# Kernel tuning notes

Hardware: AMD Instinct MI355X
Metric: run time of the kernel (lower is better)

Reference implementation:

```python
import jax, jax.numpy as jnp
import numpy as np

N, D, K = 32768, 64, 8192

def setup_inputs() -> dict:
    key = jax.random.key(0)
    k1, k2 = jax.random.split(key)
    x = jax.random.normal(k1, (N, D), dtype=jnp.float32)
    w = jax.random.normal(k2, (D, K), dtype=jnp.float32)  # codebook: (embedding_dim, num_embeddings)
    return {"x": x, "w": w}

def reference(x, w):
    distances = (
        jnp.sum(x * x, axis=1, keepdims=True)
        - 2.0 * (x @ w)
        + jnp.sum(w * w, axis=0, keepdims=True)
    )  # [N, K]
    encoding_indices = jnp.argmin(distances, axis=1)  # [N] (argmax of -distances)
    # quantize: embedding_lookup on w^T  -> [N, D]
    quantized = jnp.take(w.T, encoding_indices, axis=0)
    return quantized
```

## Files before the change

kernel.cpp:

```cpp
#include <hip/hip_runtime.h>
#include <hip/hip_bf16.h>
#include <hip/hip_fp16.h>
#include <cstdint>
#include <cstddef>

#define NROWS 32768
#define DDIM  64
#define KDIM  8192
#define DELTA 1.25f

typedef float  f32x4 __attribute__((ext_vector_type(4)));
typedef short  s16x8 __attribute__((ext_vector_type(8)));
typedef unsigned long long u64;


__device__ __forceinline__ uint32_t fmono(float f) {
    uint32_t u = __float_as_uint(f);
    return (u & 0x80000000u) ? ~u : (u | 0x80000000u);
}


__global__ void __launch_bounds__(256)
vq_prep(const float* __restrict__ w, const float* __restrict__ x,
        ushort* __restrict__ wtb, float* __restrict__ wt,
        float4* __restrict__ wt4, float* __restrict__ wsq,
        ushort* __restrict__ xb) {
    __shared__ float tile[64][65];
    const int t = threadIdx.x, wv = t >> 6, lane = t & 63;
    const int l15 = lane & 15, l4 = (lane >> 4) & 3;

    if (blockIdx.x < KDIM / 64) {
        const int bid = blockIdx.x;
        const int kbase = bid * 64;
#pragma unroll
        for (int it = 0; it < 16; ++it) {
            int d = it * 4 + wv;
            tile[lane][d] = w[(size_t)d * KDIM + kbase + lane];
        }
        __syncthreads();
#pragma unroll
        for (int h = 0; h < 2; ++h) {
            s16x8 c;
#pragma unroll
            for (int e = 0; e < 8; ++e) {
                float v = -2.0f * tile[wv * 16 + l15][h * 32 + l4 * 8 + e];
                __hip_bfloat16 hb = __float2bfloat16(v);
                c[e] = *(short*)&hb;
            }
            ((s16x8*)wtb)[(size_t)(bid * 4 + wv) * 128 + h * 64 + lane] = c;
        }
#pragma unroll
        for (int it = 0; it < 16; ++it) {
            int kk = it * 4 + wv;
            wt[(size_t)(kbase + kk) * DDIM + lane] = tile[kk][lane];
        }
#pragma unroll
        for (int it = 0; it < 4; ++it) {
            int i = wv * 4 + it;
            float4 v;
            v.x = tile[lane][i * 4 + 0];
            v.y = tile[lane][i * 4 + 1];
            v.z = tile[lane][i * 4 + 2];
            v.w = tile[lane][i * 4 + 3];
            wt4[(size_t)i * KDIM + kbase + lane] = v;
        }
        if (wv == 0) {
            float s = 0.f;
#pragma unroll
            for (int d = 0; d < DDIM; ++d) {
                float v = tile[lane][d];
                s = fmaf(v, v, s);
            }
            wsq[kbase + lane] = s;
        }
    } else {
        const int bid = blockIdx.x - KDIM / 64;
        const int r = bid * 64 + wv * 16 + l15;
#pragma unroll
        for (int h = 0; h < 2; ++h) {
            const float* src = &x[(size_t)r * DDIM + h * 32 + l4 * 8];
            float4 a = *(const float4*)src;
            float4 b = *(const float4*)(src + 4);
            float fv[8] = {a.x, a.y, a.z, a.w, b.x, b.y, b.z, b.w};
            s16x8 c;
#pragma unroll
            for (int e = 0; e < 8; ++e) {
                __hip_bfloat16 hb = __float2bfloat16(fv[e]);
                c[e] = *(short*)&hb;
            }
            ((s16x8*)xb)[(size_t)(bid * 4 + wv) * 128 + h * 64 + lane] = c;
        }
    }
}

__global__ void __launch_bounds__(256)
vq_scoreA(const ushort* __restrict__ xb, const ushort* __restrict__ wb,
          const float* __restrict__ wsq, ushort* __restrict__ lsub) {
    const int t = threadIdx.x, wv = t >> 6, lane = t & 63;
    const int l15 = lane & 15, l4 = lane >> 4;
    const int rbase = (blockIdx.x & 255) * 128;
    const int kg    = (blockIdx.x >> 8) * 4 + wv;
    const int kbase = kg * 256;

    const s16x8* xs  = (const s16x8*)xb;
    const s16x8* wsx = (const s16x8*)wb;

    s16x8 bfrag[8][2];
#pragma unroll
    for (int rt = 0; rt < 8; ++rt)
#pragma unroll
        for (int h = 0; h < 2; ++h)
            bfrag[rt][h] = xs[(size_t)((rbase >> 4) + rt) * 128 + h * 64 + lane];

    u64 packs[8];
#pragma unroll
    for (int rt = 0; rt < 8; ++rt) packs[rt] = 0ull;

#pragma unroll
    for (int sub = 0; sub < 4; ++sub) {
        const int kw = kbase + sub * 64;

        s16x8 afrag[4][2];
#pragma unroll
        for (int kt = 0; kt < 4; ++kt)
#pragma unroll
            for (int h = 0; h < 2; ++h)
                afrag[kt][h] = wsx[(size_t)((kw >> 4) + kt) * 128 + h * 64 + lane];

        f32x4 wq[4];
#pragma unroll
        for (int kt = 0; kt < 4; ++kt)
            wq[kt] = *(const f32x4*)&wsq[kw + kt * 16 + l4 * 4];

#pragma unroll
        for (int rt = 0; rt < 8; ++rt) {
            f32x4 acc[4];
#pragma unroll
            for (int kt = 0; kt < 4; ++kt) acc[kt] = wq[kt];
#pragma unroll
            for (int kt = 0; kt < 4; ++kt) {
                acc[kt] = __builtin_amdgcn_mfma_f32_16x16x32_bf16(afrag[kt][0], bfrag[rt][0], acc[kt], 0, 0, 0);
                acc[kt] = __builtin_amdgcn_mfma_f32_16x16x32_bf16(afrag[kt][1], bfrag[rt][1], acc[kt], 0, 0, 0);
            }
            float g0 = fminf(fminf(acc[0][0], acc[0][1]), acc[0][2]);
            float g1 = fminf(fminf(acc[0][3], acc[1][0]), acc[1][1]);
            float g2 = fminf(fminf(acc[1][2], acc[1][3]), acc[2][0]);
            float g3 = fminf(fminf(acc[2][1], acc[2][2]), acc[2][3]);
            float g4 = fminf(fminf(acc[3][0], acc[3][1]), acc[3][2]);
            float h0 = fminf(fminf(g0, g1), g2);
            float h1 = fminf(fminf(g3, g4), acc[3][3]);
            float m  = fminf(h0, h1);
            m = fminf(m, __shfl_xor(m, 16));
            m = fminf(m, __shfl_xor(m, 32));
            __half hh = __float2half(m);
            packs[rt] |= (u64)(*(ushort*)&hh) << (16 * sub);
        }
    }

    if (l4 == 0) {
#pragma unroll
        for (int rt = 0; rt < 8; ++rt)
            *(u64*)&lsub[(size_t)(rbase + rt * 16 + l15) * 128 + kg * 4] = packs[rt];
    }
}

__global__ void __launch_bounds__(64)
vq_finish(const float* __restrict__ x, const float4* __restrict__ wt4,
          const float* __restrict__ wt, const float* __restrict__ wsq,
          const ushort* __restrict__ lsub, float* __restrict__ out) {
    const int lane = threadIdx.x;
    const int row  = blockIdx.x;

    ushort2 us = ((const ushort2*)(lsub + (size_t)row * 128))[lane];
    float v0 = __half2float(*(__half*)&us.x);
    float v1 = __half2float(*(__half*)&us.y);
    float m = fminf(v0, v1);
#pragma unroll
    for (int o = 1; o < 64; o <<= 1) m = fminf(m, __shfl_xor(m, o));
    const float thr = m + DELTA;
    u64 b0 = __ballot(v0 <= thr);
    u64 b1 = __ballot(v1 <= thr);

    float xs[64];
    const float4* xp = (const float4*)(x + (size_t)row * DDIM);
#pragma unroll
    for (int i = 0; i < 16; ++i) {
        float4 v = xp[i];
        xs[4 * i + 0] = v.x;
        xs[4 * i + 1] = v.y;
        xs[4 * i + 2] = v.z;
        xs[4 * i + 3] = v.w;
    }

    u64 best = ~0ull;
#pragma unroll
    for (int half = 0; half < 2; ++half) {
        u64 b = half ? b1 : b0;
        while (b) {
            int s = __ffsll(b) - 1;
            b &= b - 1;
            const int kk = (s * 2 + half) * 64 + lane;
            float qq = wsq[kk];
            const float4* wr = wt4 + kk;
            float a0 = 0.f, a1 = 0.f, a2 = 0.f, a3 = 0.f;
#pragma unroll
            for (int i = 0; i < 16; ++i) {
                float4 wv4 = wr[(size_t)i * KDIM];
                a0 = fmaf(xs[4 * i + 0], wv4.x, a0);
                a1 = fmaf(xs[4 * i + 1], wv4.y, a1);
                a2 = fmaf(xs[4 * i + 2], wv4.z, a2);
                a3 = fmaf(xs[4 * i + 3], wv4.w, a3);
            }
            float dot = (a0 + a1) + (a2 + a3);
            float sc  = fmaf(-2.f, dot, qq);
            u64 key = ((u64)fmono(sc) << 32) | (unsigned)kk;
            best = (key < best) ? key : best;
        }
    }
#pragma unroll
    for (int sh = 1; sh < 64; sh <<= 1) {
        u64 o = __shfl_xor(best, sh);
        best = (o < best) ? o : best;
    }
    const int bk = (int)(best & 0xFFFFFFFFull);
    out[(size_t)row * DDIM + lane] = wt[(size_t)bk * DDIM + lane];
}


#define BR 128
#define BK 128
#define DPH 32
typedef float v2f __attribute__((ext_vector_type(2)));

__global__ void fb_prep(const float* __restrict__ w, float* __restrict__ wt,
                        float* __restrict__ wsq) {
    int k = blockIdx.x * blockDim.x + threadIdx.x;
    if (k >= KDIM) return;
    float s = 0.f;
#pragma unroll
    for (int d = 0; d < DDIM; ++d) {
        float v = w[(size_t)d * KDIM + k];
        wt[(size_t)k * DDIM + d] = v;
        s = fmaf(v, v, s);
    }
    wsq[k] = s;
}
__global__ void fb_init(u64* __restrict__ keys) {
    int i = blockIdx.x * blockDim.x + threadIdx.x;
    if (i < NROWS) keys[i] = ~0ull;
}
__global__ void __launch_bounds__(256, 4)
fb_gemm(const float* __restrict__ x, const float* __restrict__ w,
        const float* __restrict__ wsq, u64* __restrict__ keys) {
    __shared__ float xT[DPH][BR];
    __shared__ float wl[DPH][BK];
    const int kblk  = blockIdx.x & (KDIM / BK - 1);
    const int rbase = (blockIdx.x >> 6) * BR;
    const int kbase = kblk * BK;
    const int t     = threadIdx.x;
    const int wave = t >> 6, lane = t & 63;
    const int rg = lane >> 3, cg = lane & 7;
    const int xoff = (wave >> 1) * 64 + rg * 8;
    const int coff = (wave & 1) * 64 + cg * 8;
    v2f acc[8][4];
#pragma unroll
    for (int i = 0; i < 8; ++i)
#pragma unroll
        for (int j = 0; j < 4; ++j) acc[i][j] = (v2f)(0.f);
#pragma unroll
    for (int p = 0; p < 2; ++p) {
        {
            const int row = t & 127, dgrp = t >> 7;
#pragma unroll
            for (int it = 0; it < 4; ++it) {
                const int dl = (dgrp + it * 2) * 4;
                float4 v = *(const float4*)&x[(size_t)(rbase + row) * DDIM + p * DPH + dl];
                xT[dl + 0][row] = v.x; xT[dl + 1][row] = v.y;
                xT[dl + 2][row] = v.z; xT[dl + 3][row] = v.w;
            }
        }
        {
#pragma unroll
            for (int it = 0; it < 4; ++it) {
                const int o4 = t + it * 256;
                const int dl = o4 >> 5, c4 = (o4 & 31) << 2;
                float4 v = *(const float4*)&w[(size_t)(p * DPH + dl) * KDIM + kbase + c4];
                *(float4*)&wl[dl][c4] = v;
            }
        }
        __syncthreads();
#pragma unroll 4
        for (int d = 0; d < DPH; ++d) {
            float4 xa = *(const float4*)&xT[d][xoff];
            float4 xb = *(const float4*)&xT[d][xoff + 4];
            float4 wa = *(const float4*)&wl[d][coff];
            float4 wb = *(const float4*)&wl[d][coff + 4];
            v2f wv0 = {wa.x, wa.y}, wv1 = {wa.z, wa.w};
            v2f wv2 = {wb.x, wb.y}, wv3 = {wb.z, wb.w};
            float xrr[8] = {xa.x, xa.y, xa.z, xa.w, xb.x, xb.y, xb.z, xb.w};
#pragma unroll
            for (int i = 0; i < 8; ++i) {
                v2f xsV = {xrr[i], xrr[i]};
                acc[i][0] = __builtin_elementwise_fma(xsV, wv0, acc[i][0]);
                acc[i][1] = __builtin_elementwise_fma(xsV, wv1, acc[i][1]);
                acc[i][2] = __builtin_elementwise_fma(xsV, wv2, acc[i][2]);
                acc[i][3] = __builtin_elementwise_fma(xsV, wv3, acc[i][3]);
            }
        }
        __syncthreads();
    }
    const int kc = kbase + coff;
    float4 qa = *(const float4*)&wsq[kc];
    float4 qb = *(const float4*)&wsq[kc + 4];
    v2f q2[4] = {{qa.x, qa.y}, {qa.z, qa.w}, {qb.x, qb.y}, {qb.z, qb.w}};
    const v2f neg2 = {-2.f, -2.f};
#pragma unroll
    for (int i = 0; i < 8; ++i) {
        float sc[8];
#pragma unroll
        for (int jj = 0; jj < 4; ++jj) {
            v2f s2 = __builtin_elementwise_fma(neg2, acc[i][jj], q2[jj]);
            sc[2 * jj] = s2.x; sc[2 * jj + 1] = s2.y;
        }
        float bestv = sc[0]; int bj = 0;
#pragma unroll
        for (int j = 1; j < 8; ++j)
            if (sc[j] < bestv) { bestv = sc[j]; bj = j; }
        u64 key = ((u64)fmono(bestv) << 32) | (unsigned)(kc + bj);
        u64 o;
        o = __shfl_xor(key, 1); key = (o < key) ? o : key;
        o = __shfl_xor(key, 2); key = (o < key) ? o : key;
        o = __shfl_xor(key, 4); key = (o < key) ? o : key;
        if (cg == 0) atomicMin(&keys[rbase + xoff + i], key);
    }
}
__global__ void fb_gather(const u64* __restrict__ keys,
                          const float* __restrict__ wt,
                          float* __restrict__ out) {
    int t = blockIdx.x * blockDim.x + threadIdx.x;
    if (t >= NROWS * DDIM) return;
    int row = t >> 6;
    int d   = t & 63;
    int k   = (int)(keys[row] & 0xFFFFFFFFull);
    out[t] = wt[(size_t)k * DDIM + d];
}


extern "C" void kernel_launch(void* const* d_in, const int* in_sizes, int n_in,
                              void* d_out, int out_size, void* d_ws, size_t ws_size,
                              hipStream_t stream) {
    const float* x = (const float*)d_in[0];
    const float* w = (const float*)d_in[1];
    float* out = (float*)d_out;

    char* ws = (char*)d_ws;
    const size_t OFF_WTB  = 0;
    const size_t OFF_WSQ  = 1048576;
    const size_t OFF_XB   = 1081344;
    const size_t OFF_WT   = 5275648;
    const size_t OFF_WT4  = 7372800;
    const size_t OFF_LSUB = 9469952;
    const size_t NEED     = 17858560;

    if (ws_size >= NEED) {
        ushort* wtb  = (ushort*)(ws + OFF_WTB);
        float*  wsq  = (float*)(ws + OFF_WSQ);
        ushort* xbb  = (ushort*)(ws + OFF_XB);
        float*  wt   = (float*)(ws + OFF_WT);
        float4* wt4  = (float4*)(ws + OFF_WT4);
        ushort* lsub = (ushort*)(ws + OFF_LSUB);

        vq_prep<<<KDIM / 64 + NROWS / 64, 256, 0, stream>>>(w, x, wtb, wt, wt4, wsq, xbb);
        vq_scoreA<<<(NROWS / 128) * 8, 256, 0, stream>>>(xbb, wtb, wsq, lsub);
        vq_finish<<<NROWS, 64, 0, stream>>>(x, wt4, wt, wsq, lsub, out);
    } else {
        float* wt  = (float*)ws;
        float* wsq = (float*)(ws + 2097152);
        u64*   keys = (u64*)(ws + 2129920);
        fb_prep<<<KDIM / 256, 256, 0, stream>>>(w, wt, wsq);
        fb_init<<<NROWS / 256, 256, 0, stream>>>(keys);
        fb_gemm<<<(NROWS / BR) * (KDIM / BK), 256, 0, stream>>>(x, w, wsq, keys);
        fb_gather<<<(NROWS * DDIM) / 256, 256, 0, stream>>>(keys, wt, out);
    }
}
```

Before: 80.48 us.

## Switch scoring GEMM from 16x16x32 to 32x32x16 bf16 MFMA with matching layouts

The bf16 operand layouts produced by the prep kernel are changed to 32-row fragments, and the scoring kernel now uses 32x32x16 MFMA instructions instead of 16x16x32. Each wave computes 32x32 tiles, which reduces operand fragment loads per FLOP and removes one cross-lane shuffle step in the per-row min reduction. The cost is larger accumulator vectors, which raise register pressure, and a different accumulator-to-row mapping that both kernels must agree on.

```diff
diff --git a/kernel.cpp b/kernel.cpp
--- a/kernel.cpp
+++ b/kernel.cpp
@@ -9,8 +9,9 @@
 #define KDIM  8192
 #define DELTA 1.25f
 
-typedef float  f32x4 __attribute__((ext_vector_type(4)));
-typedef short  s16x8 __attribute__((ext_vector_type(8)));
+typedef float  f32x4  __attribute__((ext_vector_type(4)));
+typedef float  f32x16 __attribute__((ext_vector_type(16)));
+typedef short  s16x8  __attribute__((ext_vector_type(8)));
 typedef unsigned long long u64;
 
 
@@ -27,7 +28,7 @@
         ushort* __restrict__ xb) {
     __shared__ float tile[64][65];
     const int t = threadIdx.x, wv = t >> 6, lane = t & 63;
-    const int l15 = lane & 15, l4 = (lane >> 4) & 3;
+    const int c31 = lane & 31, l5 = lane >> 5;
 
     if (blockIdx.x < KDIM / 64) {
         const int bid = blockIdx.x;
@@ -39,15 +40,17 @@
         }
         __syncthreads();
 #pragma unroll
-        for (int h = 0; h < 2; ++h) {
+        for (int it = 0; it < 2; ++it) {
+            const int L = wv * 2 + it;
+            const int kt2 = L >> 2, h = L & 3;
             s16x8 c;
 #pragma unroll
             for (int e = 0; e < 8; ++e) {
-                float v = -2.0f * tile[wv * 16 + l15][h * 32 + l4 * 8 + e];
+                float v = -2.0f * tile[kt2 * 32 + c31][h * 16 + l5 * 8 + e];
                 __hip_bfloat16 hb = __float2bfloat16(v);
                 c[e] = *(short*)&hb;
             }
-            ((s16x8*)wtb)[(size_t)(bid * 4 + wv) * 128 + h * 64 + lane] = c;
+            ((s16x8*)wtb)[(size_t)(bid * 2 + kt2) * 256 + h * 64 + lane] = c;
         }
 #pragma unroll
         for (int it = 0; it < 16; ++it) {
@@ -75,10 +78,12 @@
         }
     } else {
         const int bid = blockIdx.x - KDIM / 64;
-        const int r = bid * 64 + wv * 16 + l15;
-#pragma unroll
-        for (int h = 0; h < 2; ++h) {
-            const float* src = &x[(size_t)r * DDIM + h * 32 + l4 * 8];
+#pragma unroll
+        for (int it = 0; it < 2; ++it) {
+            const int L = wv * 2 + it;
+            const int rt2 = L >> 2, h = L & 3;
+            const int r = bid * 64 + rt2 * 32 + c31;
+            const float* src = &x[(size_t)r * DDIM + h * 16 + l5 * 8];
             float4 a = *(const float4*)src;
             float4 b = *(const float4*)(src + 4);
             float fv[8] = {a.x, a.y, a.z, a.w, b.x, b.y, b.z, b.w};
@@ -88,7 +93,7 @@
                 __hip_bfloat16 hb = __float2bfloat16(fv[e]);
                 c[e] = *(short*)&hb;
             }
-            ((s16x8*)xb)[(size_t)(bid * 4 + wv) * 128 + h * 64 + lane] = c;
+            ((s16x8*)xb)[(size_t)(bid * 2 + rt2) * 256 + h * 64 + lane] = c;
         }
     }
 }
@@ -97,7 +102,7 @@
 vq_scoreA(const ushort* __restrict__ xb, const ushort* __restrict__ wb,
           const float* __restrict__ wsq, ushort* __restrict__ lsub) {
     const int t = threadIdx.x, wv = t >> 6, lane = t & 63;
-    const int l15 = lane & 15, l4 = lane >> 4;
+    const int c31 = lane & 31, l5 = lane >> 5;
     const int rbase = (blockIdx.x & 255) * 128;
     const int kg    = (blockIdx.x >> 8) * 4 + wv;
     const int kbase = kg * 256;
@@ -105,62 +110,69 @@
     const s16x8* xs  = (const s16x8*)xb;
     const s16x8* wsx = (const s16x8*)wb;
 
-    s16x8 bfrag[8][2];
-#pragma unroll
-    for (int rt = 0; rt < 8; ++rt)
-#pragma unroll
-        for (int h = 0; h < 2; ++h)
-            bfrag[rt][h] = xs[(size_t)((rbase >> 4) + rt) * 128 + h * 64 + lane];
-
-    u64 packs[8];
-#pragma unroll
-    for (int rt = 0; rt < 8; ++rt) packs[rt] = 0ull;
+    s16x8 bfrag[4][4];
+#pragma unroll
+    for (int rt = 0; rt < 4; ++rt)
+#pragma unroll
+        for (int h = 0; h < 4; ++h)
+            bfrag[rt][h] = xs[(size_t)((rbase >> 5) + rt) * 256 + h * 64 + lane];
+
+    u64 packs[4];
+#pragma unroll
+    for (int rt = 0; rt < 4; ++rt) packs[rt] = 0ull;
 
 #pragma unroll
     for (int sub = 0; sub < 4; ++sub) {
         const int kw = kbase + sub * 64;
-
-        s16x8 afrag[4][2];
-#pragma unroll
-        for (int kt = 0; kt < 4; ++kt)
-#pragma unroll
-            for (int h = 0; h < 2; ++h)
-                afrag[kt][h] = wsx[(size_t)((kw >> 4) + kt) * 128 + h * 64 + lane];
-
-        f32x4 wq[4];
-#pragma unroll
-        for (int kt = 0; kt < 4; ++kt)
-            wq[kt] = *(const f32x4*)&wsq[kw + kt * 16 + l4 * 4];
-
-#pragma unroll
-        for (int rt = 0; rt < 8; ++rt) {
-            f32x4 acc[4];
-#pragma unroll
-            for (int kt = 0; kt < 4; ++kt) acc[kt] = wq[kt];
-#pragma unroll
-            for (int kt = 0; kt < 4; ++kt) {
-                acc[kt] = __builtin_amdgcn_mfma_f32_16x16x32_bf16(afrag[kt][0], bfrag[rt][0], acc[kt], 0, 0, 0);
-                acc[kt] = __builtin_amdgcn_mfma_f32_16x16x32_bf16(afrag[kt][1], bfrag[rt][1], acc[kt], 0, 0, 0);
-            }
-            float g0 = fminf(fminf(acc[0][0], acc[0][1]), acc[0][2]);
-            float g1 = fminf(fminf(acc[0][3], acc[1][0]), acc[1][1]);
-            float g2 = fminf(fminf(acc[1][2], acc[1][3]), acc[2][0]);
-            float g3 = fminf(fminf(acc[2][1], acc[2][2]), acc[2][3]);
-            float g4 = fminf(fminf(acc[3][0], acc[3][1]), acc[3][2]);
-            float h0 = fminf(fminf(g0, g1), g2);
-            float h1 = fminf(fminf(g3, g4), acc[3][3]);
-            float m  = fminf(h0, h1);
-            m = fminf(m, __shfl_xor(m, 16));
+        float m2[2][4];
+
+#pragma unroll
+        for (int kt = 0; kt < 2; ++kt) {
+            s16x8 af[4];
+#pragma unroll
+            for (int h = 0; h < 4; ++h)
+                af[h] = wsx[(size_t)((kw >> 5) + kt) * 256 + h * 64 + lane];
+
+            f32x4 wq[4];
+#pragma unroll
+            for (int q = 0; q < 4; ++q)
+                wq[q] = *(const f32x4*)&wsq[kw + kt * 32 + q * 8 + 4 * l5];
+
+#pragma unroll
+            for (int rt = 0; rt < 4; ++rt) {
+                f32x16 acc;
+#pragma unroll
+                for (int q = 0; q < 4; ++q)
+#pragma unroll
+                    for (int j = 0; j < 4; ++j) acc[q * 4 + j] = wq[q][j];
+#pragma unroll
+                for (int h = 0; h < 4; ++h)
+                    acc = __builtin_amdgcn_mfma_f32_32x32x16_bf16(
+                        af[h], bfrag[rt][h], acc, 0, 0, 0);
+                float g0 = fminf(fminf(acc[0],  acc[1]),  acc[2]);
+                float g1 = fminf(fminf(acc[3],  acc[4]),  acc[5]);
+                float g2 = fminf(fminf(acc[6],  acc[7]),  acc[8]);
+                float g3 = fminf(fminf(acc[9],  acc[10]), acc[11]);
+                float g4 = fminf(fminf(acc[12], acc[13]), acc[14]);
+                float h0 = fminf(fminf(g0, g1), g2);
+                float h1 = fminf(g3, g4);
+                m2[kt][rt] = fminf(fminf(h0, h1), acc[15]);
+            }
+        }
+
+#pragma unroll
+        for (int rt = 0; rt < 4; ++rt) {
+            float m = fminf(m2[0][rt], m2[1][rt]);
             m = fminf(m, __shfl_xor(m, 32));
             __half hh = __float2half(m);
             packs[rt] |= (u64)(*(ushort*)&hh) << (16 * sub);
         }
     }
 
-    if (l4 == 0) {
-#pragma unroll
-        for (int rt = 0; rt < 8; ++rt)
-            *(u64*)&lsub[(size_t)(rbase + rt * 16 + l15) * 128 + kg * 4] = packs[rt];
+    if (lane < 32) {
+#pragma unroll
+        for (int rt = 0; rt < 4; ++rt)
+            *(u64*)&lsub[(size_t)(rbase + rt * 32 + c31) * 128 + kg * 4] = packs[rt];
     }
 }
 
```

New measurement: 81.14 us. Within noise of the previous version (+0.8%).
